# Optimization experiments

Hardware: AMD Instinct MI355X
Metric: run time of the kernel (lower is better)

## Reference

```python
import jax, jax.numpy as jnp
import numpy as np

ALPHA = 0.2  # LeakyReLU negative slope
NEG_INF = -9e15


def setup_inputs() -> dict:
    key = jax.random.key(0)
    ks = jax.random.split(key, 12)
    Nd, Nk = 8000, 2000
    Fd, Fk, H, Hh = 32, 16, 64, 8
    s = lambda fan_in: 1.0 / np.sqrt(fan_in)
    return {
        "raw_drone": jax.random.normal(ks[0], (Nd, Fd), jnp.float32),
        "raw_dock": jax.random.normal(ks[1], (Nk, Fk), jnp.float32),
        "adj": jax.random.randint(ks[2], (Nd, Nk), 0, 2, jnp.int32),
        # proj_drone / proj_dock (nn.Linear)
        "Wpd": jax.random.uniform(ks[3], (Fd, H), jnp.float32, -s(Fd), s(Fd)),
        "bpd": jnp.zeros((H,), jnp.float32),
        "Wpk": jax.random.uniform(ks[4], (Fk, H), jnp.float32, -s(Fk), s(Fk)),
        "bpk": jnp.zeros((H,), jnp.float32),
        # per-head GAT params, stacked over heads: W [Hh,H,H], attention vecs a1,a2 [Hh,H]
        "Wa": jax.random.uniform(ks[5], (Hh, H, H), jnp.float32, -s(H), s(H)),
        "a1": jax.random.uniform(ks[6], (Hh, H), jnp.float32, -s(H), s(H)),
        "a2": jax.random.uniform(ks[7], (Hh, H), jnp.float32, -s(H), s(H)),
        # feature_fusion (nn.Linear nhid*nheads -> nhid)
        "Wf": jax.random.uniform(ks[8], (Hh * H, H), jnp.float32, -s(Hh * H), s(Hh * H)),
        "bf": jnp.zeros((H,), jnp.float32),
    }


def reference(raw_drone, raw_dock, adj, Wpd, bpd, Wpk, bpk, Wa, a1, a2, Wf, bf):
    # input projections + ELU (dropout is identity in eval mode)
    h_drone = jax.nn.elu(raw_drone @ Wpd + bpd)  # [Nd, H]
    h_dock = jax.nn.elu(raw_dock @ Wpk + bpk)    # [Nk, H]

    # per-head linear transforms, vectorized over heads
    Whd = jnp.einsum("nd,hdf->hnf", h_drone, Wa)  # [Hh, Nd, F]
    Whk = jnp.einsum("kd,hdf->hkf", h_dock, Wa)   # [Hh, Nk, F]

    # additive GAT scores: e[h,n,k] = LeakyReLU(a1_h . Whd[h,n] + a2_h . Whk[h,k])
    sd = jnp.einsum("hnf,hf->hn", Whd, a1)  # [Hh, Nd]
    sk = jnp.einsum("hkf,hf->hk", Whk, a2)  # [Hh, Nk]
    e = jax.nn.leaky_relu(sd[:, :, None] + sk[:, None, :], negative_slope=ALPHA)

    # adjacency-masked softmax over dock axis
    e = jnp.where(adj[None, :, :] > 0, e, NEG_INF)
    attn = jax.nn.softmax(e, axis=-1)  # [Hh, Nd, Nk]

    # aggregate dock features, ELU (concat=True), concat heads
    hp = jax.nn.elu(jnp.einsum("hnk,hkf->hnf", attn, Whk))  # [Hh, Nd, F]
    Nd = hp.shape[1]
    hp = jnp.transpose(hp, (1, 0, 2)).reshape(Nd, -1)  # [Nd, Hh*F]

    out_drone = hp @ Wf + bf
    return (out_drone, h_dock)
```

## Files before the change

kernel.cpp:

```cpp
#include <hip/hip_runtime.h>
#include <stdint.h>

#define Nd 8000
#define Nk 2000
#define FD 32
#define FK 16
#define HD 64
#define NH 8
#define KP 2048
#define NKB 64
#define LOG2E 1.44269504088896f
#define NSLOPE 0.2f

typedef float f4 __attribute__((ext_vector_type(4)));
typedef short s16x8 __attribute__((ext_vector_type(8)));
typedef unsigned int u32;
typedef unsigned short u16;
typedef unsigned int u4v __attribute__((ext_vector_type(4)));

#define WS_WHKB   0
#define WS_SK     2097152
#define WS_SD     2162688
#define WS_ADJB   2418688
#define WS_WFT    4466688
#define WS_HP     4532224

__device__ inline u16 f2bf_rne(float f){
  u32 u = __float_as_uint(f);
  u32 r = u + 0x7fffu + ((u >> 16) & 1u);
  return (u16)(r >> 16);
}
__device__ inline float elu1(float x){
  return x > 0.f ? x : (__builtin_amdgcn_exp2f(x * LOG2E) - 1.f);
}

__global__ __launch_bounds__(256) void k_whk(const float* __restrict__ rdock,
                                             const float* __restrict__ Wpk,
                                             const float* __restrict__ bpk,
                                             const float* __restrict__ Wa,
                                             const float* __restrict__ a2,
                                             const float* __restrict__ Wf,
                                             float* __restrict__ out_hdock,
                                             u16* __restrict__ whkB,
                                             float* __restrict__ sk,
                                             u16* __restrict__ wfT){
  int kt = blockIdx.x, h = blockIdx.y;
  int t = threadIdx.x;
  __shared__ float hs[32 * 65];
  __shared__ float part[32 * 8];
  __shared__ u16 ts[64 * 32];

  if (h == 1) {
    int id = kt * 256 + t;
    #pragma unroll
    for (int i = 0; i < 2; ++i) {
      int idx = id * 2 + i;
      int j = idx >> 9, k = idx & 511;
      wfT[idx] = f2bf_rne(Wf[k * HD + j]);
    }
  }
  {
    int r = t >> 3, f0 = (t & 7) * 8;
    int gk = kt * 32 + r;
    float v[8];
    if (gk < Nk) {
      #pragma unroll
      for (int q = 0; q < 8; ++q) v[q] = bpk[f0 + q];
      for (int j = 0; j < FK; ++j) {
        float x = rdock[gk * FK + j];
        #pragma unroll
        for (int q = 0; q < 8; ++q) v[q] += x * Wpk[j * HD + f0 + q];
      }
      #pragma unroll
      for (int q = 0; q < 8; ++q) v[q] = elu1(v[q]);
      if (h == 0) {
        #pragma unroll
        for (int q = 0; q < 8; ++q) out_hdock[gk * HD + f0 + q] = v[q];
      }
    } else {
      #pragma unroll
      for (int q = 0; q < 8; ++q) v[q] = 0.f;
    }
    #pragma unroll
    for (int q = 0; q < 8; ++q) hs[r * 65 + f0 + q] = v[q];
  }
  __syncthreads();
  {
    int kl = t & 31, fq = t >> 5;
    float acc[8];
    #pragma unroll
    for (int j = 0; j < 8; ++j) acc[j] = 0.f;
    for (int d = 0; d < HD; ++d) {
      float hv = hs[kl * 65 + d];
      const float* wr = Wa + (h * HD + d) * HD + fq * 8;
      #pragma unroll
      for (int j = 0; j < 8; ++j) acc[j] += hv * wr[j];
    }
    float ps = 0.f;
    #pragma unroll
    for (int j = 0; j < 8; ++j) ps += acc[j] * a2[h * HD + fq * 8 + j];
    part[kl * 8 + fq] = ps;
    #pragma unroll
    for (int j = 0; j < 8; ++j)
      ts[(fq * 8 + j) * 32 + kl] = f2bf_rne(acc[j]);
  }
  __syncthreads();
  if (t < 32) {
    float s = 0.f;
    #pragma unroll
    for (int q = 0; q < 8; ++q) s += part[t * 8 + q];
    sk[h * KP + kt * 32 + t] = s * LOG2E;
  }
  {
    int cc = t >> 6, lane = t & 63, g = (t >> 4) & 3, c16 = t & 15;
    int f = cc * 16 + c16;
    u4v val = *(const u4v*)&ts[f * 32 + g * 8];
    *(u4v*)(whkB + (((h * NKB + kt) * 4 + cc) * 64 + lane) * 8) = val;
  }
}

__global__ __launch_bounds__(256) void k_dsd(const float* __restrict__ rdrone,
                                             const float* __restrict__ Wpd,
                                             const float* __restrict__ bpd,
                                             const float* __restrict__ Wa,
                                             const float* __restrict__ a1,
                                             float* __restrict__ sd){
  __shared__ float wa1[NH * HD];
  int t = threadIdx.x;
  #pragma unroll
  for (int i = 0; i < 2; ++i) {
    int idx = t + i * 256;
    int h = idx >> 6, d = idx & 63;
    float s = 0.f;
    for (int f = 0; f < HD; ++f) s += Wa[(h * HD + d) * HD + f] * a1[h * HD + f];
    wa1[idx] = s;
  }
  __syncthreads();
  int r4 = t >> 6, d = t & 63;
  for (int rr = 0; rr < 4; ++rr) {
    int n = blockIdx.x * 16 + r4 * 4 + rr;
    float acc = bpd[d];
    for (int j = 0; j < FD; ++j) acc += rdrone[n * FD + j] * Wpd[j * HD + d];
    float hd = elu1(acc);
    #pragma unroll
    for (int h = 0; h < NH; ++h) {
      float v = hd * wa1[h * HD + d];
      v += __shfl_xor(v, 1);  v += __shfl_xor(v, 2);  v += __shfl_xor(v, 4);
      v += __shfl_xor(v, 8);  v += __shfl_xor(v, 16); v += __shfl_xor(v, 32);
      if (d == 0) sd[h * Nd + n] = v * LOG2E;
    }
  }
}

__global__ __launch_bounds__(256) void k_adjb(const int* __restrict__ adj,
                                              unsigned long long* __restrict__ adjb){
  int wv = threadIdx.x >> 6, lane = threadIdx.x & 63;
  int n = blockIdx.x * 4 + wv;
  for (int c = 0; c < 32; ++c) {
    int k = c * 64 + lane;
    int v = (k < Nk) ? adj[n * Nk + k] : 0;
    unsigned long long m = __ballot(v != 0);
    if (lane == 0) adjb[n * 32 + c] = m;
  }
}

__global__ __launch_bounds__(256) void k_attn(const float* __restrict__ sd,
                                              const float* __restrict__ sk,
                                              const u16* __restrict__ whkB,
                                              const u32* __restrict__ adjb,
                                              u16* __restrict__ hp){
  int h = blockIdx.y, nt = blockIdx.x;
  int t = threadIdx.x;
  int w = t >> 6, lane = t & 63, g = lane >> 4, c16 = lane & 15;
  int r0 = nt * 128 + w * 32;
  __shared__ u16 ldshp[128 * 64];

  int rowA[2]; float sdv[2];
  #pragma unroll
  for (int m = 0; m < 2; ++m) {
    rowA[m] = min(r0 + m * 16 + c16, Nd - 1);
    sdv[m] = sd[h * Nd + rowA[m]];
  }
  f4 acc[2][4], accd[2];
  #pragma unroll
  for (int m = 0; m < 2; ++m) {
    accd[m] = (f4){0.f, 0.f, 0.f, 0.f};
    #pragma unroll
    for (int cc = 0; cc < 4; ++cc) acc[m][cc] = (f4){0.f, 0.f, 0.f, 0.f};
  }
  s16x8 onesf = (s16x8)(short)((c16 == 0) ? 0x3F80 : 0);

  const u16* bb = whkB + h * (NKB * 4 * 64 * 8);
  const float* skh = sk + h * KP;
  const u32* ap0 = adjb + rowA[0] * 64;
  const u32* ap1 = adjb + rowA[1] * 64;

  for (int kb4 = 0; kb4 < 16; ++kb4) {
    u4v aw0 = *(const u4v*)(ap0 + kb4 * 4);
    u4v aw1 = *(const u4v*)(ap1 + kb4 * 4);
    #pragma unroll
    for (int u = 0; u < 4; ++u) {
      int kb = kb4 * 4 + u;
      const float* sp = skh + kb * 32 + g * 8;
      f4 s0 = *(const f4*)sp;
      f4 s1 = *(const f4*)(sp + 4);
      const u16* bp = bb + kb * 2048 + lane * 8;
      s16x8 b0 = *(const s16x8*)(bp);
      s16x8 b1 = *(const s16x8*)(bp + 512);
      s16x8 b2 = *(const s16x8*)(bp + 1024);
      s16x8 b3 = *(const s16x8*)(bp + 1536);
      u32 awm0 = aw0[u], awm1 = aw1[u];
      union { s16x8 v; u32 d[4]; } af[2];
      #pragma unroll
      for (int m = 0; m < 2; ++m) {
        u32 ab = ((m ? awm1 : awm0) >> (g * 8)) & 0xffu;
        float p[8];
        #pragma unroll
        for (int e = 0; e < 8; ++e) {
          float x = sdv[m] + (e < 4 ? s0[e] : s1[e - 4]);
          x = fmaxf(x, x * NSLOPE);
          float pe = __builtin_amdgcn_exp2f(x);
          p[e] = (ab & (1u << e)) ? pe : 0.f;
        }
        #pragma unroll
        for (int jj = 0; jj < 4; ++jj)
          asm("v_cvt_pk_bf16_f32 %0, %1, %2"
              : "=v"(af[m].d[jj]) : "v"(p[2 * jj]), "v"(p[2 * jj + 1]));
      }
      #pragma unroll
      for (int m = 0; m < 2; ++m) {
        accd[m]   = __builtin_amdgcn_mfma_f32_16x16x32_bf16(af[m].v, onesf, accd[m], 0, 0, 0);
        acc[m][0] = __builtin_amdgcn_mfma_f32_16x16x32_bf16(af[m].v, b0, acc[m][0], 0, 0, 0);
        acc[m][1] = __builtin_amdgcn_mfma_f32_16x16x32_bf16(af[m].v, b1, acc[m][1], 0, 0, 0);
        acc[m][2] = __builtin_amdgcn_mfma_f32_16x16x32_bf16(af[m].v, b2, acc[m][2], 0, 0, 0);
        acc[m][3] = __builtin_amdgcn_mfma_f32_16x16x32_bf16(af[m].v, b3, acc[m][3], 0, 0, 0);
      }
    }
  }

  #pragma unroll
  for (int m = 0; m < 2; ++m) {
    #pragma unroll
    for (int j = 0; j < 4; ++j) {
      float den = __shfl(accd[m][j], lane & 48);
      int row = r0 + m * 16 + g * 4 + j;
      float linv = (row < Nd && den > 0.f) ? 1.f / den : 0.f;
      #pragma unroll
      for (int cc = 0; cc < 4; ++cc) {
        float o = acc[m][cc][j] * linv;
        ldshp[(w * 32 + m * 16 + g * 4 + j) * 64 + cc * 16 + c16] = f2bf_rne(elu1(o));
      }
    }
  }
  __syncthreads();
  {
    int r = t >> 1, half = t & 1;
    int row = nt * 128 + r;
    if (row < Nd) {
      u16* dst = hp + row * 512 + h * 64 + half * 32;
      const u16* src = ldshp + r * 64 + half * 32;
      *(u4v*)(dst)      = *(const u4v*)(src);
      *(u4v*)(dst + 8)  = *(const u4v*)(src + 8);
      *(u4v*)(dst + 16) = *(const u4v*)(src + 16);
      *(u4v*)(dst + 24) = *(const u4v*)(src + 24);
    }
  }
}

__global__ __launch_bounds__(256) void k_out(const u16* __restrict__ hp,
                                             const u16* __restrict__ wfT,
                                             const float* __restrict__ bfv,
                                             float* __restrict__ out){
  int t = threadIdx.x;
  int w = t >> 6, lane = t & 63, g = lane >> 4, c16 = lane & 15;
  int r0 = blockIdx.x * 64 + w * 16;
  f4 acc[4];
  #pragma unroll
  for (int cc = 0; cc < 4; ++cc) acc[cc] = (f4){0.f, 0.f, 0.f, 0.f};
  const u16* ap = hp + (r0 + c16) * 512 + g * 8;
  for (int kb = 0; kb < 16; ++kb) {
    s16x8 a = *(const s16x8*)(ap + kb * 32);
    #pragma unroll
    for (int cc = 0; cc < 4; ++cc) {
      s16x8 b = *(const s16x8*)(wfT + (cc * 16 + c16) * 512 + kb * 32 + g * 8);
      acc[cc] = __builtin_amdgcn_mfma_f32_16x16x32_bf16(a, b, acc[cc], 0, 0, 0);
    }
  }
  #pragma unroll
  for (int cc = 0; cc < 4; ++cc) {
    float bias = bfv[cc * 16 + c16];
    #pragma unroll
    for (int j = 0; j < 4; ++j) {
      int row = r0 + g * 4 + j;
      out[row * HD + cc * 16 + c16] = acc[cc][j] + bias;
    }
  }
}

extern "C" void kernel_launch(void* const* d_in, const int* in_sizes, int n_in,
                              void* d_out, int out_size, void* d_ws, size_t ws_size,
                              hipStream_t stream) {
  const float* raw_drone = (const float*)d_in[0];
  const float* raw_dock  = (const float*)d_in[1];
  const int*   adj       = (const int*)d_in[2];
  const float* Wpd = (const float*)d_in[3];
  const float* bpd = (const float*)d_in[4];
  const float* Wpk = (const float*)d_in[5];
  const float* bpk = (const float*)d_in[6];
  const float* Wa  = (const float*)d_in[7];
  const float* a1  = (const float*)d_in[8];
  const float* a2  = (const float*)d_in[9];
  const float* Wf  = (const float*)d_in[10];
  const float* bfb = (const float*)d_in[11];
  float* out = (float*)d_out;
  float* out_hdock = out + Nd * HD;

  char* ws = (char*)d_ws;
  u16*   whkB = (u16*)(ws + WS_WHKB);
  float* skv  = (float*)(ws + WS_SK);
  float* sdv  = (float*)(ws + WS_SD);
  u32*   adjb = (u32*)(ws + WS_ADJB);
  u16*   wfT  = (u16*)(ws + WS_WFT);
  u16*   hp   = (u16*)(ws + WS_HP);

  k_whk <<<dim3(64, 8), 256, 0, stream>>>(raw_dock, Wpk, bpk, Wa, a2, Wf,
                                          out_hdock, whkB, skv, wfT);
  k_dsd <<<500, 256, 0, stream>>>(raw_drone, Wpd, bpd, Wa, a1, sdv);
  k_adjb<<<2000, 256, 0, stream>>>(adj, (unsigned long long*)adjb);
  k_attn<<<dim3(63, 8), 256, 0, stream>>>(sdv, skv, whkB, adjb, hp);
  k_out <<<125, 256, 0, stream>>>(hp, wfT, bfb, out);
}
```

Measured before the change: 113.7 us.

## Merge preprocessing kernels, prefetch B tiles in attention, split output GEMM

The three independent preprocessing kernels (adjacency bit-packing, dock projection/Whk, drone score) become one launch that dispatches on block index, removing two launch gaps and letting the work run concurrently. In the attention kernel, the next k-block's bf16 B fragments are software-prefetched into registers, and the LeakyReLU/exp2 math is vectorized with a bitwise mask instead of a select. The output GEMM now gives each wave one 16-column slice across 500 blocks instead of four slices across 125 blocks, raising parallelism. The changes cost more registers in the attention loop and one redundant wrap-around prefetch.

Result: slower. 126.6 us (+11.3%).

```diff
diff --git a/kernel.cpp b/kernel.cpp
--- a/kernel.cpp
+++ b/kernel.cpp
@@ -34,133 +34,139 @@
   return x > 0.f ? x : (__builtin_amdgcn_exp2f(x * LOG2E) - 1.f);
 }
 
-__global__ __launch_bounds__(256) void k_whk(const float* __restrict__ rdock,
-                                             const float* __restrict__ Wpk,
-                                             const float* __restrict__ bpk,
-                                             const float* __restrict__ Wa,
-                                             const float* __restrict__ a2,
-                                             const float* __restrict__ Wf,
-                                             float* __restrict__ out_hdock,
-                                             u16* __restrict__ whkB,
-                                             float* __restrict__ sk,
-                                             u16* __restrict__ wfT){
-  int kt = blockIdx.x, h = blockIdx.y;
+__global__ __launch_bounds__(256) void k_prep(const float* __restrict__ rdrone,
+                                              const float* __restrict__ rdock,
+                                              const int*   __restrict__ adj,
+                                              const float* __restrict__ Wpd,
+                                              const float* __restrict__ bpd,
+                                              const float* __restrict__ Wpk,
+                                              const float* __restrict__ bpk,
+                                              const float* __restrict__ Wa,
+                                              const float* __restrict__ a1,
+                                              const float* __restrict__ a2,
+                                              const float* __restrict__ Wf,
+                                              float* __restrict__ out_hdock,
+                                              u16* __restrict__ whkB,
+                                              float* __restrict__ sk,
+                                              float* __restrict__ sd,
+                                              unsigned long long* __restrict__ adjb,
+                                              u16* __restrict__ wfT){
+  __shared__ __align__(16) char smem[13440];
+  int b = blockIdx.x;
   int t = threadIdx.x;
-  __shared__ float hs[32 * 65];
-  __shared__ float part[32 * 8];
-  __shared__ u16 ts[64 * 32];
-
-  if (h == 1) {
-    int id = kt * 256 + t;
+
+  if (b < 2000) {
+    int wv = t >> 6, lane = t & 63;
+    int n = b * 4 + wv;
+    for (int c = 0; c < 32; ++c) {
+      int k = c * 64 + lane;
+      int v = (k < Nk) ? adj[n * Nk + k] : 0;
+      unsigned long long m = __ballot(v != 0);
+      if (lane == 0) adjb[n * 32 + c] = m;
+    }
+    return;
+  }
+  if (b < 2512) {
+    int idx = b - 2000;
+    int kt = idx & 63, h = idx >> 6;
+    float* hs   = (float*)smem;
+    float* part = (float*)(smem + 8320);
+    u16*   ts   = (u16*)(smem + 9344);
+    if (h == 1) {
+      int id = kt * 256 + t;
+      #pragma unroll
+      for (int i = 0; i < 2; ++i) {
+        int ix = id * 2 + i;
+        int j = ix >> 9, k = ix & 511;
+        wfT[ix] = f2bf_rne(Wf[k * HD + j]);
+      }
+    }
+    {
+      int r = t >> 3, f0 = (t & 7) * 8;
+      int gk = kt * 32 + r;
+      float v[8];
+      if (gk < Nk) {
+        #pragma unroll
+        for (int q = 0; q < 8; ++q) v[q] = bpk[f0 + q];
+        for (int j = 0; j < FK; ++j) {
+          float x = rdock[gk * FK + j];
+          #pragma unroll
+          for (int q = 0; q < 8; ++q) v[q] += x * Wpk[j * HD + f0 + q];
+        }
+        #pragma unroll
+        for (int q = 0; q < 8; ++q) v[q] = elu1(v[q]);
+        if (h == 0) {
+          #pragma unroll
+          for (int q = 0; q < 8; ++q) out_hdock[gk * HD + f0 + q] = v[q];
+        }
+      } else {
+        #pragma unroll
+        for (int q = 0; q < 8; ++q) v[q] = 0.f;
+      }
+      #pragma unroll
+      for (int q = 0; q < 8; ++q) hs[r * 65 + f0 + q] = v[q];
+    }
+    __syncthreads();
+    {
+      int kl = t & 31, fq = t >> 5;
+      float acc[8];
+      #pragma unroll
+      for (int j = 0; j < 8; ++j) acc[j] = 0.f;
+      for (int d = 0; d < HD; ++d) {
+        float hv = hs[kl * 65 + d];
+        const float* wr = Wa + (h * HD + d) * HD + fq * 8;
+        #pragma unroll
+        for (int j = 0; j < 8; ++j) acc[j] += hv * wr[j];
+      }
+      float ps = 0.f;
+      #pragma unroll
+      for (int j = 0; j < 8; ++j) ps += acc[j] * a2[h * HD + fq * 8 + j];
+      part[kl * 8 + fq] = ps;
+      #pragma unroll
+      for (int j = 0; j < 8; ++j)
+        ts[(fq * 8 + j) * 32 + kl] = f2bf_rne(acc[j]);
+    }
+    __syncthreads();
+    if (t < 32) {
+      float s = 0.f;
+      #pragma unroll
+      for (int q = 0; q < 8; ++q) s += part[t * 8 + q];
+      sk[h * KP + kt * 32 + t] = s * LOG2E;
+    }
+    {
+      int cc = t >> 6, lane = t & 63, g = (t >> 4) & 3, c16 = t & 15;
+      int f = cc * 16 + c16;
+      u4v val = *(const u4v*)&ts[f * 32 + g * 8];
+      *(u4v*)(whkB + (((h * NKB + kt) * 4 + cc) * 64 + lane) * 8) = val;
+    }
+    return;
+  }
+  {
+    int bid = b - 2512;
+    float* wa1 = (float*)smem;
     #pragma unroll
     for (int i = 0; i < 2; ++i) {
-      int idx = id * 2 + i;
-      int j = idx >> 9, k = idx & 511;
-      wfT[idx] = f2bf_rne(Wf[k * HD + j]);
-    }
-  }
-  {
-    int r = t >> 3, f0 = (t & 7) * 8;
-    int gk = kt * 32 + r;
-    float v[8];
-    if (gk < Nk) {
-      #pragma unroll
-      for (int q = 0; q < 8; ++q) v[q] = bpk[f0 + q];
-      for (int j = 0; j < FK; ++j) {
-        float x = rdock[gk * FK + j];
-        #pragma unroll
-        for (int q = 0; q < 8; ++q) v[q] += x * Wpk[j * HD + f0 + q];
-      }
-      #pragma unroll
-      for (int q = 0; q < 8; ++q) v[q] = elu1(v[q]);
-      if (h == 0) {
-        #pragma unroll
-        for (int q = 0; q < 8; ++q) out_hdock[gk * HD + f0 + q] = v[q];
-      }
-    } else {
-      #pragma unroll
-      for (int q = 0; q < 8; ++q) v[q] = 0.f;
-    }
-    #pragma unroll
-    for (int q = 0; q < 8; ++q) hs[r * 65 + f0 + q] = v[q];
-  }
-  __syncthreads();
-  {
-    int kl = t & 31, fq = t >> 5;
-    float acc[8];
-    #pragma unroll
-    for (int j = 0; j < 8; ++j) acc[j] = 0.f;
-    for (int d = 0; d < HD; ++d) {
-      float hv = hs[kl * 65 + d];
-      const float* wr = Wa + (h * HD + d) * HD + fq * 8;
-      #pragma unroll
-      for (int j = 0; j < 8; ++j) acc[j] += hv * wr[j];
-    }
-    float ps = 0.f;
-    #pragma unroll
-    for (int j = 0; j < 8; ++j) ps += acc[j] * a2[h * HD + fq * 8 + j];
-    part[kl * 8 + fq] = ps;
-    #pragma unroll
-    for (int j = 0; j < 8; ++j)
-      ts[(fq * 8 + j) * 32 + kl] = f2bf_rne(acc[j]);
-  }
-  __syncthreads();
-  if (t < 32) {
-    float s = 0.f;
-    #pragma unroll
-    for (int q = 0; q < 8; ++q) s += part[t * 8 + q];
-    sk[h * KP + kt * 32 + t] = s * LOG2E;
-  }
-  {
-    int cc = t >> 6, lane = t & 63, g = (t >> 4) & 3, c16 = t & 15;
-    int f = cc * 16 + c16;
-    u4v val = *(const u4v*)&ts[f * 32 + g * 8];
-    *(u4v*)(whkB + (((h * NKB + kt) * 4 + cc) * 64 + lane) * 8) = val;
-  }
-}
-
-__global__ __launch_bounds__(256) void k_dsd(const float* __restrict__ rdrone,
-                                             const float* __restrict__ Wpd,
-                                             const float* __restrict__ bpd,
-                                             const float* __restrict__ Wa,
-                                             const float* __restrict__ a1,
-                                             float* __restrict__ sd){
-  __shared__ float wa1[NH * HD];
-  int t = threadIdx.x;
-  #pragma unroll
-  for (int i = 0; i < 2; ++i) {
-    int idx = t + i * 256;
-    int h = idx >> 6, d = idx & 63;
-    float s = 0.f;
-    for (int f = 0; f < HD; ++f) s += Wa[(h * HD + d) * HD + f] * a1[h * HD + f];
-    wa1[idx] = s;
-  }
-  __syncthreads();
-  int r4 = t >> 6, d = t & 63;
-  for (int rr = 0; rr < 4; ++rr) {
-    int n = blockIdx.x * 16 + r4 * 4 + rr;
-    float acc = bpd[d];
-    for (int j = 0; j < FD; ++j) acc += rdrone[n * FD + j] * Wpd[j * HD + d];
-    float hd = elu1(acc);
-    #pragma unroll
-    for (int h = 0; h < NH; ++h) {
-      float v = hd * wa1[h * HD + d];
-      v += __shfl_xor(v, 1);  v += __shfl_xor(v, 2);  v += __shfl_xor(v, 4);
-      v += __shfl_xor(v, 8);  v += __shfl_xor(v, 16); v += __shfl_xor(v, 32);
-      if (d == 0) sd[h * Nd + n] = v * LOG2E;
-    }
-  }
-}
-
-__global__ __launch_bounds__(256) void k_adjb(const int* __restrict__ adj,
-                                              unsigned long long* __restrict__ adjb){
-  int wv = threadIdx.x >> 6, lane = threadIdx.x & 63;
-  int n = blockIdx.x * 4 + wv;
-  for (int c = 0; c < 32; ++c) {
-    int k = c * 64 + lane;
-    int v = (k < Nk) ? adj[n * Nk + k] : 0;
-    unsigned long long m = __ballot(v != 0);
-    if (lane == 0) adjb[n * 32 + c] = m;
+      int ix = t + i * 256;
+      int h = ix >> 6, d = ix & 63;
+      float s = 0.f;
+      for (int f = 0; f < HD; ++f) s += Wa[(h * HD + d) * HD + f] * a1[h * HD + f];
+      wa1[ix] = s;
+    }
+    __syncthreads();
+    int r4 = t >> 6, d = t & 63;
+    for (int rr = 0; rr < 4; ++rr) {
+      int n = bid * 16 + r4 * 4 + rr;
+      float acc = bpd[d];
+      for (int j = 0; j < FD; ++j) acc += rdrone[n * FD + j] * Wpd[j * HD + d];
+      float hd = elu1(acc);
+      #pragma unroll
+      for (int h = 0; h < NH; ++h) {
+        float v = hd * wa1[h * HD + d];
+        v += __shfl_xor(v, 1);  v += __shfl_xor(v, 2);  v += __shfl_xor(v, 4);
+        v += __shfl_xor(v, 8);  v += __shfl_xor(v, 16); v += __shfl_xor(v, 32);
+        if (d == 0) sd[h * Nd + n] = v * LOG2E;
+      }
+    }
   }
 }
 
@@ -195,32 +201,49 @@
   const u32* ap0 = adjb + rowA[0] * 64;
   const u32* ap1 = adjb + rowA[1] * 64;
 
+  s16x8 cb0, cb1, cb2, cb3;
+  {
+    const u16* bp = bb + lane * 8;
+    cb0 = *(const s16x8*)(bp);
+    cb1 = *(const s16x8*)(bp + 512);
+    cb2 = *(const s16x8*)(bp + 1024);
+    cb3 = *(const s16x8*)(bp + 1536);
+  }
+
   for (int kb4 = 0; kb4 < 16; ++kb4) {
     u4v aw0 = *(const u4v*)(ap0 + kb4 * 4);
     u4v aw1 = *(const u4v*)(ap1 + kb4 * 4);
     #pragma unroll
     for (int u = 0; u < 4; ++u) {
       int kb = kb4 * 4 + u;
+      const u16* np = bb + ((kb + 1) & 63) * 2048 + lane * 8;
+      s16x8 nb0 = *(const s16x8*)(np);
+      s16x8 nb1 = *(const s16x8*)(np + 512);
+      s16x8 nb2 = *(const s16x8*)(np + 1024);
+      s16x8 nb3 = *(const s16x8*)(np + 1536);
+
       const float* sp = skh + kb * 32 + g * 8;
       f4 s0 = *(const f4*)sp;
       f4 s1 = *(const f4*)(sp + 4);
-      const u16* bp = bb + kb * 2048 + lane * 8;
-      s16x8 b0 = *(const s16x8*)(bp);
-      s16x8 b1 = *(const s16x8*)(bp + 512);
-      s16x8 b2 = *(const s16x8*)(bp + 1024);
-      s16x8 b3 = *(const s16x8*)(bp + 1536);
       u32 awm0 = aw0[u], awm1 = aw1[u];
       union { s16x8 v; u32 d[4]; } af[2];
       #pragma unroll
       for (int m = 0; m < 2; ++m) {
         u32 ab = ((m ? awm1 : awm0) >> (g * 8)) & 0xffu;
+        f4 x0 = s0 + sdv[m];
+        f4 x1 = s1 + sdv[m];
+        x0 = __builtin_elementwise_max(x0, x0 * NSLOPE);
+        x1 = __builtin_elementwise_max(x1, x1 * NSLOPE);
         float p[8];
         #pragma unroll
+        for (int e = 0; e < 4; ++e) {
+          p[e]     = __builtin_amdgcn_exp2f(x0[e]);
+          p[e + 4] = __builtin_amdgcn_exp2f(x1[e]);
+        }
+        #pragma unroll
         for (int e = 0; e < 8; ++e) {
-          float x = sdv[m] + (e < 4 ? s0[e] : s1[e - 4]);
-          x = fmaxf(x, x * NSLOPE);
-          float pe = __builtin_amdgcn_exp2f(x);
-          p[e] = (ab & (1u << e)) ? pe : 0.f;
+          int mk = __builtin_amdgcn_sbfe(ab, e, 1);
+          p[e] = __uint_as_float(__float_as_uint(p[e]) & (u32)mk);
         }
         #pragma unroll
         for (int jj = 0; jj < 4; ++jj)
@@ -230,11 +253,12 @@
       #pragma unroll
       for (int m = 0; m < 2; ++m) {
         accd[m]   = __builtin_amdgcn_mfma_f32_16x16x32_bf16(af[m].v, onesf, accd[m], 0, 0, 0);
-        acc[m][0] = __builtin_amdgcn_mfma_f32_16x16x32_bf16(af[m].v, b0, acc[m][0], 0, 0, 0);
-        acc[m][1] = __builtin_amdgcn_mfma_f32_16x16x32_bf16(af[m].v, b1, acc[m][1], 0, 0, 0);
-        acc[m][2] = __builtin_amdgcn_mfma_f32_16x16x32_bf16(af[m].v, b2, acc[m][2], 0, 0, 0);
-        acc[m][3] = __builtin_amdgcn_mfma_f32_16x16x32_bf16(af[m].v, b3, acc[m][3], 0, 0, 0);
-      }
+        acc[m][0] = __builtin_amdgcn_mfma_f32_16x16x32_bf16(af[m].v, cb0, acc[m][0], 0, 0, 0);
+        acc[m][1] = __builtin_amdgcn_mfma_f32_16x16x32_bf16(af[m].v, cb1, acc[m][1], 0, 0, 0);
+        acc[m][2] = __builtin_amdgcn_mfma_f32_16x16x32_bf16(af[m].v, cb2, acc[m][2], 0, 0, 0);
+        acc[m][3] = __builtin_amdgcn_mfma_f32_16x16x32_bf16(af[m].v, cb3, acc[m][3], 0, 0, 0);
+      }
+      cb0 = nb0; cb1 = nb1; cb2 = nb2; cb3 = nb3;
     }
   }
 
@@ -273,28 +297,20 @@
                                              float* __restrict__ out){
   int t = threadIdx.x;
   int w = t >> 6, lane = t & 63, g = lane >> 4, c16 = lane & 15;
-  int r0 = blockIdx.x * 64 + w * 16;
-  f4 acc[4];
-  #pragma unroll
-  for (int cc = 0; cc < 4; ++cc) acc[cc] = (f4){0.f, 0.f, 0.f, 0.f};
+  int r0 = blockIdx.x * 16;
+  f4 acc = (f4){0.f, 0.f, 0.f, 0.f};
   const u16* ap = hp + (r0 + c16) * 512 + g * 8;
+  const u16* bp = wfT + (w * 16 + c16) * 512 + g * 8;
+  #pragma unroll 4
   for (int kb = 0; kb < 16; ++kb) {
     s16x8 a = *(const s16x8*)(ap + kb * 32);
-    #pragma unroll
-    for (int cc = 0; cc < 4; ++cc) {
-      s16x8 b = *(const s16x8*)(wfT + (cc * 16 + c16) * 512 + kb * 32 + g * 8);
-      acc[cc] = __builtin_amdgcn_mfma_f32_16x16x32_bf16(a, b, acc[cc], 0, 0, 0);
-    }
-  }
+    s16x8 b = *(const s16x8*)(bp + kb * 32);
+    acc = __builtin_amdgcn_mfma_f32_16x16x32_bf16(a, b, acc, 0, 0, 0);
+  }
+  float bias = bfv[w * 16 + c16];
   #pragma unroll
-  for (int cc = 0; cc < 4; ++cc) {
-    float bias = bfv[cc * 16 + c16];
-    #pragma unroll
-    for (int j = 0; j < 4; ++j) {
-      int row = r0 + g * 4 + j;
-      out[row * HD + cc * 16 + c16] = acc[cc][j] + bias;
-    }
-  }
+  for (int j = 0; j < 4; ++j)
+    out[(r0 + g * 4 + j) * HD + w * 16 + c16] = acc[j] + bias;
 }
 
 extern "C" void kernel_launch(void* const* d_in, const int* in_sizes, int n_in,
@@ -323,10 +339,9 @@
   u16*   wfT  = (u16*)(ws + WS_WFT);
   u16*   hp   = (u16*)(ws + WS_HP);
 
-  k_whk <<<dim3(64, 8), 256, 0, stream>>>(raw_dock, Wpk, bpk, Wa, a2, Wf,
-                                          out_hdock, whkB, skv, wfT);
-  k_dsd <<<500, 256, 0, stream>>>(raw_drone, Wpd, bpd, Wa, a1, sdv);
-  k_adjb<<<2000, 256, 0, stream>>>(adj, (unsigned long long*)adjb);
+  k_prep<<<3012, 256, 0, stream>>>(raw_drone, raw_dock, adj, Wpd, bpd, Wpk, bpk,
+                                   Wa, a1, a2, Wf, out_hdock, whkB, skv, sdv,
+                                   (unsigned long long*)adjb, wfT);
   k_attn<<<dim3(63, 8), 256, 0, stream>>>(sdv, skv, whkB, adjb, hp);
-  k_out <<<125, 256, 0, stream>>>(hp, wfT, bfb, out);
-}
+  k_out <<<500, 256, 0, stream>>>(hp, wfT, bfb, out);
+}
```
